# Optimization experiments

Measured on AMD Instinct MI355X. Metric: run time of the kernel, lower is better.

## Reference

```python
import jax, jax.numpy as jnp
import numpy as np

H = 64
EPS = 1e-5


def _lstm_layer(x, w_ih, w_hh, b_ih, b_hh):
    """Single LSTM layer, batch_first input x: [B, T, I]. PyTorch gate order i,f,g,o."""
    B, T, _ = x.shape
    # precompute input contributions for all timesteps: [B, T, 4H]
    xw = jnp.einsum('bti,gi->btg', x, w_ih) + (b_ih + b_hh)
    xw = jnp.swapaxes(xw, 0, 1)  # [T, B, 4H] for scan over time

    def step(carry, xw_t):
        h, c = carry
        gates = xw_t + h @ w_hh.T  # [B, 4H]
        i, f, g, o = jnp.split(gates, 4, axis=-1)
        i = jax.nn.sigmoid(i)
        f = jax.nn.sigmoid(f)
        g = jnp.tanh(g)
        o = jax.nn.sigmoid(o)
        c = f * c + i * g
        h = o * jnp.tanh(c)
        return (h, c), h

    h0 = jnp.zeros((B, H), x.dtype)
    (_, _), hs = jax.lax.scan(step, (h0, h0), xw)
    return jnp.swapaxes(hs, 0, 1)  # [B, T, H]


def setup_inputs() -> dict:
    key = jax.random.key(0)
    ks = jax.random.split(key, 16)
    B, T, F = 4096, 256, 32
    s = 1.0 / np.sqrt(H)  # PyTorch LSTM init scale
    inp = {
        'x': jax.random.normal(ks[0], (B, T, F), jnp.float32),
        'w_ih0': jax.random.uniform(ks[1], (4 * H, F), jnp.float32, -s, s),
        'w_hh0': jax.random.uniform(ks[2], (4 * H, H), jnp.float32, -s, s),
        'b_ih0': jax.random.uniform(ks[3], (4 * H,), jnp.float32, -s, s),
        'b_hh0': jax.random.uniform(ks[4], (4 * H,), jnp.float32, -s, s),
        'w_ih1': jax.random.uniform(ks[5], (4 * H, H), jnp.float32, -s, s),
        'w_hh1': jax.random.uniform(ks[6], (4 * H, H), jnp.float32, -s, s),
        'b_ih1': jax.random.uniform(ks[7], (4 * H,), jnp.float32, -s, s),
        'b_hh1': jax.random.uniform(ks[8], (4 * H,), jnp.float32, -s, s),
        'ln_g': jnp.ones((H,), jnp.float32),
        'ln_b': jnp.zeros((H,), jnp.float32),
        'w1': jax.random.uniform(ks[9], (64, H), jnp.float32, -s, s),
        'b1': jax.random.uniform(ks[10], (64,), jnp.float32, -s, s),
        'w2': jax.random.uniform(ks[11], (1, 64), jnp.float32, -0.125, 0.125),
        'b2': jax.random.uniform(ks[12], (1,), jnp.float32, -0.125, 0.125),
    }
    return inp


def reference(x, w_ih0, w_hh0, b_ih0, b_hh0, w_ih1, w_hh1, b_ih1, b_hh1,
              ln_g, ln_b, w1, b1, w2, b2):
    out0 = _lstm_layer(x, w_ih0, w_hh0, b_ih0, b_hh0)      # [B, T, H]
    out1 = _lstm_layer(out0, w_ih1, w_hh1, b_ih1, b_hh1)   # [B, T, H]
    last = out1[:, -1, :]                                   # [B, H]
    # LayerNorm
    mu = jnp.mean(last, axis=-1, keepdims=True)
    var = jnp.mean(jnp.square(last - mu), axis=-1, keepdims=True)
    ln = (last - mu) * jax.lax.rsqrt(var + EPS) * ln_g + ln_b
    # MLP head
    h = jax.nn.relu(ln @ w1.T + b1)
    y = h @ w2.T + b2                                       # [B, 1]
    return y[:, 0]
```

## Files before the change

### kernel.cpp

```cpp
#include <hip/hip_runtime.h>

#define TSEQ 256
#define FIN  32
#define HID  64

#define LOG2E    1.4426950408889634f
#define TWOLOG2E 2.8853900817779268f

typedef _Float16 f16x8 __attribute__((ext_vector_type(8)));
typedef __fp16   h16x2 __attribute__((ext_vector_type(2)));
typedef float    f32x4 __attribute__((ext_vector_type(4)));

#if __has_builtin(__builtin_amdgcn_exp2f)
__device__ __forceinline__ float fast_exp2(float x) { return __builtin_amdgcn_exp2f(x); }
#else
extern "C" __device__ float __ocml_native_exp2_f32(float);
__device__ __forceinline__ float fast_exp2(float x) { return __ocml_native_exp2_f32(x); }
#endif

#define BAR_LDS() do { asm volatile("s_waitcnt lgkmcnt(0)" ::: "memory"); \
                       __builtin_amdgcn_s_barrier(); } while (0)

__device__ __forceinline__ float wsum(float v) {
    #pragma unroll
    for (int off = 32; off > 0; off >>= 1) v += __shfl_xor(v, off, 64);
    return v;
}

__device__ __forceinline__ float lstm_cell(const f32x4 g, float& c) {
    float ei = fast_exp2(g[0]);
    float ef = fast_exp2(g[1]);
    float yg = fast_exp2(g[2]);
    float eo = fast_exp2(g[3]);
    float t1 = 1.0f + ei;
    float t2 = 1.0f + ef;
    float p  = t1 * (yg + 1.0f);
    float r  = __builtin_amdgcn_rcpf(p * t2);
    float ig = (yg - 1.0f) * t2 * r;
    float sf = p * r;
    c = fmaf(sf, c, ig);
    float cc = __builtin_amdgcn_fmed3f(c, -15.0f, 15.0f);
    float yc = fast_exp2(TWOLOG2E * cc);
    return (yc - 1.0f) * __builtin_amdgcn_rcpf((1.0f + eo) * (yc + 1.0f));
}

__global__ __launch_bounds__(1024, 4)
void lstm_fused(const float* __restrict__ x,
                const float* __restrict__ w_ih0, const float* __restrict__ w_hh0,
                const float* __restrict__ b_ih0, const float* __restrict__ b_hh0,
                const float* __restrict__ w_ih1, const float* __restrict__ w_hh1,
                const float* __restrict__ b_ih1, const float* __restrict__ b_hh1,
                const float* __restrict__ ln_g, const float* __restrict__ ln_b,
                const float* __restrict__ w1, const float* __restrict__ b1,
                const float* __restrict__ w2, const float* __restrict__ b2,
                float* __restrict__ out)
{
    __shared__ __align__(16) _Float16 H0[2][16][72];
    __shared__ __align__(16) _Float16 H1[2][16][72];
    __shared__ __align__(16) float HF[16][68];
    __shared__ __align__(16) float LNB[16][64];

    const int tid  = threadIdx.x;
    const int wave = tid >> 6;
    const int lane = tid & 63;
    const int q    = lane >> 4;
    const int lm   = lane & 15;
    const int q8   = q * 8;
    const int b0   = blockIdx.x * 16;

    const bool isA = wave < 8;
    const int  wt  = wave & 7;
    const int  T0  = 2 * wt, T1 = T0 + 1;
    const int  np0  = T0 * 16 + lm;
    const int  np1  = T1 * 16 + lm;
    const int  row0 = (np0 & 3) * 64 + (np0 >> 2);
    const int  row1 = (np1 & 3) * 64 + (np1 >> 2);
    const int  d0 = T0 * 4 + q;
    const int  d1 = T1 * 4 + q;
    const float wsc = ((lm & 3) == 2) ? TWOLOG2E : -LOG2E;

    f16x8 wf[8];
    f32x4 bias0, bias1;
    if (isA) {
        const float* p0 = w_ih0 + row0 * FIN + q8;
        const float* p1 = w_hh0 + row0 * HID + q8;
        const float* p2 = w_hh0 + row0 * HID + 32 + q8;
        const float* p3 = w_ih0 + row1 * FIN + q8;
        const float* p4 = w_hh0 + row1 * HID + q8;
        const float* p5 = w_hh0 + row1 * HID + 32 + q8;
        #pragma unroll
        for (int j = 0; j < 8; ++j) {
            wf[0][j] = (_Float16)(wsc * p0[j]);
            wf[1][j] = (_Float16)(wsc * p1[j]);
            wf[2][j] = (_Float16)(wsc * p2[j]);
            wf[3][j] = (_Float16)(wsc * p3[j]);
            wf[4][j] = (_Float16)(wsc * p4[j]);
            wf[5][j] = (_Float16)(wsc * p5[j]);
        }
        #pragma unroll
        for (int r = 0; r < 4; ++r) {
            const float s = (r == 2) ? TWOLOG2E : -LOG2E;
            bias0[r] = s * (b_ih0[r * 64 + d0] + b_hh0[r * 64 + d0]);
            bias1[r] = s * (b_ih0[r * 64 + d1] + b_hh0[r * 64 + d1]);
        }
    } else {
        const float* p0 = w_ih1 + row0 * HID + q8;
        const float* p1 = w_ih1 + row0 * HID + 32 + q8;
        const float* p2 = w_hh1 + row0 * HID + q8;
        const float* p3 = w_hh1 + row0 * HID + 32 + q8;
        const float* p4 = w_ih1 + row1 * HID + q8;
        const float* p5 = w_ih1 + row1 * HID + 32 + q8;
        const float* p6 = w_hh1 + row1 * HID + q8;
        const float* p7 = w_hh1 + row1 * HID + 32 + q8;
        #pragma unroll
        for (int j = 0; j < 8; ++j) {
            wf[0][j] = (_Float16)(wsc * p0[j]);
            wf[1][j] = (_Float16)(wsc * p1[j]);
            wf[2][j] = (_Float16)(wsc * p2[j]);
            wf[3][j] = (_Float16)(wsc * p3[j]);
            wf[4][j] = (_Float16)(wsc * p4[j]);
            wf[5][j] = (_Float16)(wsc * p5[j]);
            wf[6][j] = (_Float16)(wsc * p6[j]);
            wf[7][j] = (_Float16)(wsc * p7[j]);
        }
        #pragma unroll
        for (int r = 0; r < 4; ++r) {
            const float s = (r == 2) ? TWOLOG2E : -LOG2E;
            bias0[r] = s * (b_ih1[r * 64 + d0] + b_hh1[r * 64 + d0]);
            bias1[r] = s * (b_ih1[r * 64 + d1] + b_hh1[r * 64 + d1]);
        }
    }

    const float* xp = x + (size_t)(b0 + lm) * TSEQ * FIN + q8;
    f32x4 xfa, xfb;
    if (isA) {
        xfa = *reinterpret_cast<const f32x4*>(xp);
        xfb = *reinterpret_cast<const f32x4*>(xp + 4);
    }

    for (int i = tid; i < 2 * 16 * 72; i += 1024) {
        ((_Float16*)H0)[i] = (_Float16)0.0f;
        ((_Float16*)H1)[i] = (_Float16)0.0f;
    }
    float c0a = 0.0f, c0b = 0.0f, c1a = 0.0f, c1b = 0.0f;
    float lastB0 = 0.0f, lastB1 = 0.0f;
    __syncthreads();

#define MFMA __builtin_amdgcn_mfma_f32_16x16x32_f16
#define INTERVAL(P, DO_A, DO_B, DO_XL, XI)                                          \
    {                                                                               \
        if (isA) {                                                                  \
            f16x8 xcur;                                                             \
            {                                                                       \
                h16x2 c0_ = __builtin_amdgcn_cvt_pkrtz(xfa[0], xfa[1]);             \
                h16x2 c1_ = __builtin_amdgcn_cvt_pkrtz(xfa[2], xfa[3]);             \
                h16x2 c2_ = __builtin_amdgcn_cvt_pkrtz(xfb[0], xfb[1]);             \
                h16x2 c3_ = __builtin_amdgcn_cvt_pkrtz(xfb[2], xfb[3]);             \
                xcur[0] = (_Float16)c0_[0]; xcur[1] = (_Float16)c0_[1];             \
                xcur[2] = (_Float16)c1_[0]; xcur[3] = (_Float16)c1_[1];             \
                xcur[4] = (_Float16)c2_[0]; xcur[5] = (_Float16)c2_[1];             \
                xcur[6] = (_Float16)c3_[0]; xcur[7] = (_Float16)c3_[1];             \
            }                                                                       \
            if (DO_XL) {                                                            \
                xfa = *reinterpret_cast<const f32x4*>(xp + (size_t)(XI) * FIN);     \
                xfb = *reinterpret_cast<const f32x4*>(xp + (size_t)(XI) * FIN + 4); \
            }                                                                       \
            if (DO_A) {                                                             \
                f32x4 a0 = bias0, a1 = bias1;                                       \
                  \
                a0 = MFMA(wf[0], xcur, a0, 0, 0, 0);                                \
                a1 = MFMA(wf[3], xcur, a1, 0, 0, 0);                                \
                f16x8 rh0a = *reinterpret_cast<const f16x8*>(&H0[(P) ^ 1][lm][q8]);      \
                f16x8 rh0b = *reinterpret_cast<const f16x8*>(&H0[(P) ^ 1][lm][32 + q8]); \
                a0 = MFMA(wf[1], rh0a, a0, 0, 0, 0);                                \
                a1 = MFMA(wf[4], rh0a, a1, 0, 0, 0);                                \
                a0 = MFMA(wf[2], rh0b, a0, 0, 0, 0);                                \
                a1 = MFMA(wf[5], rh0b, a1, 0, 0, 0);                                \
                float hv0 = lstm_cell(a0, c0a);                                     \
                float hv1 = lstm_cell(a1, c0b);                                     \
                H0[P][lm][d0] = (_Float16)hv0;                                      \
                H0[P][lm][d1] = (_Float16)hv1;                                      \
            }                                                                       \
        } else if (DO_B) {                                                          \
                           \
            f16x8 rh0a = *reinterpret_cast<const f16x8*>(&H0[(P) ^ 1][lm][q8]);      \
            f16x8 rh0b = *reinterpret_cast<const f16x8*>(&H0[(P) ^ 1][lm][32 + q8]); \
            f32x4 a0 = bias0, a1 = bias1;                                           \
            a0 = MFMA(wf[0], rh0a, a0, 0, 0, 0);                                    \
            a1 = MFMA(wf[4], rh0a, a1, 0, 0, 0);                                    \
            a0 = MFMA(wf[1], rh0b, a0, 0, 0, 0);                                    \
            a1 = MFMA(wf[5], rh0b, a1, 0, 0, 0);                                    \
            f16x8 rh1a = *reinterpret_cast<const f16x8*>(&H1[P][lm][q8]);            \
            f16x8 rh1b = *reinterpret_cast<const f16x8*>(&H1[P][lm][32 + q8]);       \
            a0 = MFMA(wf[2], rh1a, a0, 0, 0, 0);                                    \
            a1 = MFMA(wf[6], rh1a, a1, 0, 0, 0);                                    \
            a0 = MFMA(wf[3], rh1b, a0, 0, 0, 0);                                    \
            a1 = MFMA(wf[7], rh1b, a1, 0, 0, 0);                                    \
            float hv0 = lstm_cell(a0, c1a);                                         \
            float hv1 = lstm_cell(a1, c1b);                                         \
            H1[(P) ^ 1][lm][d0] = (_Float16)hv0;                                    \
            H1[(P) ^ 1][lm][d1] = (_Float16)hv1;                                    \
            lastB0 = hv0; lastB1 = hv1;                                             \
        }                                                                           \
        BAR_LDS();                                                                  \
    }

    INTERVAL(0, true, false, true, 1)

    #pragma unroll 1
    for (int ii = 0; ii < 127; ++ii) {
        const int i1 = 2 * ii + 1;
        INTERVAL(1, true, true, true, i1 + 1)
        INTERVAL(0, true, true, true, i1 + 2)
    }

    INTERVAL(1, true, true, false, 0)
    INTERVAL(0, false, true, false, 0)

#undef INTERVAL
#undef MFMA

    if (!isA) {
        HF[lm][d0] = lastB0;
        HF[lm][d1] = lastB1;
    }
    __syncthreads();

    const float lngv = ln_g[lane], lnbv = ln_b[lane];
    const float b1v = b1[lane], w2v = w2[lane];
    const float* w1row = w1 + lane * 64;
    {
        float v  = HF[wave][lane];
        float mu = wsum(v) * (1.0f / 64.0f);
        float dv = v - mu;
        float var = wsum(dv * dv) * (1.0f / 64.0f);
        float ln = dv * rsqrtf(var + 1e-5f) * lngv + lnbv;
        LNB[wave][lane] = ln;
        float s = b1v;
        #pragma unroll
        for (int dd = 0; dd < 64; ++dd)
            s = fmaf(LNB[wave][dd], w1row[dd], s);
        s = fmaxf(s, 0.0f);
        float y = wsum(s * w2v);
        if (lane == 0) out[b0 + wave] = y + b2[0];
    }
}

extern "C" void kernel_launch(void* const* d_in, const int* in_sizes, int n_in,
                              void* d_out, int out_size, void* d_ws, size_t ws_size,
                              hipStream_t stream) {
    const float* x     = (const float*)d_in[0];
    const float* w_ih0 = (const float*)d_in[1];
    const float* w_hh0 = (const float*)d_in[2];
    const float* b_ih0 = (const float*)d_in[3];
    const float* b_hh0 = (const float*)d_in[4];
    const float* w_ih1 = (const float*)d_in[5];
    const float* w_hh1 = (const float*)d_in[6];
    const float* b_ih1 = (const float*)d_in[7];
    const float* b_hh1 = (const float*)d_in[8];
    const float* ln_g  = (const float*)d_in[9];
    const float* ln_b  = (const float*)d_in[10];
    const float* w1    = (const float*)d_in[11];
    const float* b1    = (const float*)d_in[12];
    const float* w2    = (const float*)d_in[13];
    const float* b2    = (const float*)d_in[14];
    lstm_fused<<<dim3(256), dim3(1024), 0, stream>>>(
        x, w_ih0, w_hh0, b_ih0, b_hh0,
        w_ih1, w_hh1, b_ih1, b_hh1,
        ln_g, ln_b, w1, b1, w2, b2, (float*)d_out);
}
```

Baseline: 365.4 us.

## Halve block to 512 threads with each wave computing four gate tiles

Reduces each block from 16 to 8 waves (4 per LSTM layer), so every wave now owns four 16-column output tiles instead of two, holding 16 f16x8 weight fragments and four cell states in registers. Fewer waves join each per-timestep barrier, which is meant to cut synchronisation cost and give each wave more independent MFMA chains to hide latency. The trade-off is a longer serial per-wave workload on the recurrent critical path, higher register pressure, and less parallelism per block with the grid size unchanged. The LayerNorm/MLP epilogue now loops so each wave handles two batch rows.

```diff
diff --git a/kernel.cpp b/kernel.cpp
--- a/kernel.cpp
+++ b/kernel.cpp
@@ -44,7 +44,7 @@
     return (yc - 1.0f) * __builtin_amdgcn_rcpf((1.0f + eo) * (yc + 1.0f));
 }
 
-__global__ __launch_bounds__(1024, 4)
+__global__ __launch_bounds__(512, 2)
 void lstm_fused(const float* __restrict__ x,
                 const float* __restrict__ w_ih0, const float* __restrict__ w_hh0,
                 const float* __restrict__ b_ih0, const float* __restrict__ b_hh0,
@@ -68,66 +68,55 @@
     const int q8   = q * 8;
     const int b0   = blockIdx.x * 16;
 
-    const bool isA = wave < 8;
-    const int  wt  = wave & 7;
-    const int  T0  = 2 * wt, T1 = T0 + 1;
-    const int  np0  = T0 * 16 + lm;
-    const int  np1  = T1 * 16 + lm;
-    const int  row0 = (np0 & 3) * 64 + (np0 >> 2);
-    const int  row1 = (np1 & 3) * 64 + (np1 >> 2);
-    const int  d0 = T0 * 4 + q;
-    const int  d1 = T1 * 4 + q;
+    const bool isA = wave < 4;
+    const int  wt  = wave & 3;
+    const int rbase = (lm & 3) * 64 + (lm >> 2);
+    const int dq0   = wt * 16 + q;
     const float wsc = ((lm & 3) == 2) ? TWOLOG2E : -LOG2E;
 
-    f16x8 wf[8];
-    f32x4 bias0, bias1;
+    f16x8 wf[16];
+    f32x4 biasv[4];
     if (isA) {
-        const float* p0 = w_ih0 + row0 * FIN + q8;
-        const float* p1 = w_hh0 + row0 * HID + q8;
-        const float* p2 = w_hh0 + row0 * HID + 32 + q8;
-        const float* p3 = w_ih0 + row1 * FIN + q8;
-        const float* p4 = w_hh0 + row1 * HID + q8;
-        const float* p5 = w_hh0 + row1 * HID + 32 + q8;
         #pragma unroll
-        for (int j = 0; j < 8; ++j) {
-            wf[0][j] = (_Float16)(wsc * p0[j]);
-            wf[1][j] = (_Float16)(wsc * p1[j]);
-            wf[2][j] = (_Float16)(wsc * p2[j]);
-            wf[3][j] = (_Float16)(wsc * p3[j]);
-            wf[4][j] = (_Float16)(wsc * p4[j]);
-            wf[5][j] = (_Float16)(wsc * p5[j]);
-        }
-        #pragma unroll
-        for (int r = 0; r < 4; ++r) {
-            const float s = (r == 2) ? TWOLOG2E : -LOG2E;
-            bias0[r] = s * (b_ih0[r * 64 + d0] + b_hh0[r * 64 + d0]);
-            bias1[r] = s * (b_ih0[r * 64 + d1] + b_hh0[r * 64 + d1]);
+        for (int t = 0; t < 4; ++t) {
+            const int row = rbase + wt * 16 + t * 4;
+            const float* p0 = w_ih0 + row * FIN + q8;
+            const float* p1 = w_hh0 + row * HID + q8;
+            const float* p2 = p1 + 32;
+            #pragma unroll
+            for (int j = 0; j < 8; ++j) {
+                wf[t * 3 + 0][j] = (_Float16)(wsc * p0[j]);
+                wf[t * 3 + 1][j] = (_Float16)(wsc * p1[j]);
+                wf[t * 3 + 2][j] = (_Float16)(wsc * p2[j]);
+            }
+            const int d = dq0 + t * 4;
+            #pragma unroll
+            for (int r = 0; r < 4; ++r) {
+                const float s = (r == 2) ? TWOLOG2E : -LOG2E;
+                biasv[t][r] = s * (b_ih0[r * 64 + d] + b_hh0[r * 64 + d]);
+            }
         }
     } else {
-        const float* p0 = w_ih1 + row0 * HID + q8;
-        const float* p1 = w_ih1 + row0 * HID + 32 + q8;
-        const float* p2 = w_hh1 + row0 * HID + q8;
-        const float* p3 = w_hh1 + row0 * HID + 32 + q8;
-        const float* p4 = w_ih1 + row1 * HID + q8;
-        const float* p5 = w_ih1 + row1 * HID + 32 + q8;
-        const float* p6 = w_hh1 + row1 * HID + q8;
-        const float* p7 = w_hh1 + row1 * HID + 32 + q8;
         #pragma unroll
-        for (int j = 0; j < 8; ++j) {
-            wf[0][j] = (_Float16)(wsc * p0[j]);
-            wf[1][j] = (_Float16)(wsc * p1[j]);
-            wf[2][j] = (_Float16)(wsc * p2[j]);
-            wf[3][j] = (_Float16)(wsc * p3[j]);
-            wf[4][j] = (_Float16)(wsc * p4[j]);
-            wf[5][j] = (_Float16)(wsc * p5[j]);
-            wf[6][j] = (_Float16)(wsc * p6[j]);
-            wf[7][j] = (_Float16)(wsc * p7[j]);
-        }
-        #pragma unroll
-        for (int r = 0; r < 4; ++r) {
-            const float s = (r == 2) ? TWOLOG2E : -LOG2E;
-            bias0[r] = s * (b_ih1[r * 64 + d0] + b_hh1[r * 64 + d0]);
-            bias1[r] = s * (b_ih1[r * 64 + d1] + b_hh1[r * 64 + d1]);
+        for (int t = 0; t < 4; ++t) {
+            const int row = rbase + wt * 16 + t * 4;
+            const float* p0 = w_ih1 + row * HID + q8;
+            const float* p1 = p0 + 32;
+            const float* p2 = w_hh1 + row * HID + q8;
+            const float* p3 = p2 + 32;
+            #pragma unroll
+            for (int j = 0; j < 8; ++j) {
+                wf[t * 4 + 0][j] = (_Float16)(wsc * p0[j]);
+                wf[t * 4 + 1][j] = (_Float16)(wsc * p1[j]);
+                wf[t * 4 + 2][j] = (_Float16)(wsc * p2[j]);
+                wf[t * 4 + 3][j] = (_Float16)(wsc * p3[j]);
+            }
+            const int d = dq0 + t * 4;
+            #pragma unroll
+            for (int r = 0; r < 4; ++r) {
+                const float s = (r == 2) ? TWOLOG2E : -LOG2E;
+                biasv[t][r] = s * (b_ih1[r * 64 + d] + b_hh1[r * 64 + d]);
+            }
         }
     }
 
@@ -138,12 +127,12 @@
         xfb = *reinterpret_cast<const f32x4*>(xp + 4);
     }
 
-    for (int i = tid; i < 2 * 16 * 72; i += 1024) {
+    for (int i = tid; i < 2 * 16 * 72; i += 512) {
         ((_Float16*)H0)[i] = (_Float16)0.0f;
         ((_Float16*)H1)[i] = (_Float16)0.0f;
     }
-    float c0a = 0.0f, c0b = 0.0f, c1a = 0.0f, c1b = 0.0f;
-    float lastB0 = 0.0f, lastB1 = 0.0f;
+    float cs0 = 0.0f, cs1 = 0.0f, cs2 = 0.0f, cs3 = 0.0f;
+    float lastB0 = 0.0f, lastB1 = 0.0f, lastB2 = 0.0f, lastB3 = 0.0f;
     __syncthreads();
 
 #define MFMA __builtin_amdgcn_mfma_f32_16x16x32_f16
@@ -166,41 +155,62 @@
                 xfb = *reinterpret_cast<const f32x4*>(xp + (size_t)(XI) * FIN + 4); \
             }                                                                       \
             if (DO_A) {                                                             \
-                f32x4 a0 = bias0, a1 = bias1;                                       \
-                  \
+                f32x4 a0 = biasv[0], a1 = biasv[1], a2 = biasv[2], a3 = biasv[3];   \
+                   \
                 a0 = MFMA(wf[0], xcur, a0, 0, 0, 0);                                \
                 a1 = MFMA(wf[3], xcur, a1, 0, 0, 0);                                \
+                a2 = MFMA(wf[6], xcur, a2, 0, 0, 0);                                \
+                a3 = MFMA(wf[9], xcur, a3, 0, 0, 0);                                \
                 f16x8 rh0a = *reinterpret_cast<const f16x8*>(&H0[(P) ^ 1][lm][q8]);      \
                 f16x8 rh0b = *reinterpret_cast<const f16x8*>(&H0[(P) ^ 1][lm][32 + q8]); \
-                a0 = MFMA(wf[1], rh0a, a0, 0, 0, 0);                                \
-                a1 = MFMA(wf[4], rh0a, a1, 0, 0, 0);                                \
-                a0 = MFMA(wf[2], rh0b, a0, 0, 0, 0);                                \
-                a1 = MFMA(wf[5], rh0b, a1, 0, 0, 0);                                \
-                float hv0 = lstm_cell(a0, c0a);                                     \
-                float hv1 = lstm_cell(a1, c0b);                                     \
-                H0[P][lm][d0] = (_Float16)hv0;                                      \
-                H0[P][lm][d1] = (_Float16)hv1;                                      \
+                a0 = MFMA(wf[1],  rh0a, a0, 0, 0, 0);                               \
+                a1 = MFMA(wf[4],  rh0a, a1, 0, 0, 0);                               \
+                a2 = MFMA(wf[7],  rh0a, a2, 0, 0, 0);                               \
+                a3 = MFMA(wf[10], rh0a, a3, 0, 0, 0);                               \
+                a0 = MFMA(wf[2],  rh0b, a0, 0, 0, 0);                               \
+                a1 = MFMA(wf[5],  rh0b, a1, 0, 0, 0);                               \
+                a2 = MFMA(wf[8],  rh0b, a2, 0, 0, 0);                               \
+                a3 = MFMA(wf[11], rh0b, a3, 0, 0, 0);                               \
+                float hv0 = lstm_cell(a0, cs0);                                     \
+                float hv1 = lstm_cell(a1, cs1);                                     \
+                float hv2 = lstm_cell(a2, cs2);                                     \
+                float hv3 = lstm_cell(a3, cs3);                                     \
+                H0[P][lm][dq0]      = (_Float16)hv0;                                \
+                H0[P][lm][dq0 + 4]  = (_Float16)hv1;                                \
+                H0[P][lm][dq0 + 8]  = (_Float16)hv2;                                \
+                H0[P][lm][dq0 + 12] = (_Float16)hv3;                                \
             }                                                                       \
         } else if (DO_B) {                                                          \
-                           \
             f16x8 rh0a = *reinterpret_cast<const f16x8*>(&H0[(P) ^ 1][lm][q8]);      \
             f16x8 rh0b = *reinterpret_cast<const f16x8*>(&H0[(P) ^ 1][lm][32 + q8]); \
-            f32x4 a0 = bias0, a1 = bias1;                                           \
-            a0 = MFMA(wf[0], rh0a, a0, 0, 0, 0);                                    \
-            a1 = MFMA(wf[4], rh0a, a1, 0, 0, 0);                                    \
-            a0 = MFMA(wf[1], rh0b, a0, 0, 0, 0);                                    \
-            a1 = MFMA(wf[5], rh0b, a1, 0, 0, 0);                                    \
+            f32x4 a0 = biasv[0], a1 = biasv[1], a2 = biasv[2], a3 = biasv[3];       \
+            a0 = MFMA(wf[0],  rh0a, a0, 0, 0, 0);                                   \
+            a1 = MFMA(wf[4],  rh0a, a1, 0, 0, 0);                                   \
+            a2 = MFMA(wf[8],  rh0a, a2, 0, 0, 0);                                   \
+            a3 = MFMA(wf[12], rh0a, a3, 0, 0, 0);                                   \
+            a0 = MFMA(wf[1],  rh0b, a0, 0, 0, 0);                                   \
+            a1 = MFMA(wf[5],  rh0b, a1, 0, 0, 0);                                   \
+            a2 = MFMA(wf[9],  rh0b, a2, 0, 0, 0);                                   \
+            a3 = MFMA(wf[13], rh0b, a3, 0, 0, 0);                                   \
             f16x8 rh1a = *reinterpret_cast<const f16x8*>(&H1[P][lm][q8]);            \
             f16x8 rh1b = *reinterpret_cast<const f16x8*>(&H1[P][lm][32 + q8]);       \
-            a0 = MFMA(wf[2], rh1a, a0, 0, 0, 0);                                    \
-            a1 = MFMA(wf[6], rh1a, a1, 0, 0, 0);                                    \
-            a0 = MFMA(wf[3], rh1b, a0, 0, 0, 0);                                    \
-            a1 = MFMA(wf[7], rh1b, a1, 0, 0, 0);                                    \
-            float hv0 = lstm_cell(a0, c1a);                                         \
-            float hv1 = lstm_cell(a1, c1b);                                         \
-            H1[(P) ^ 1][lm][d0] = (_Float16)hv0;                                    \
-            H1[(P) ^ 1][lm][d1] = (_Float16)hv1;                                    \
-            lastB0 = hv0; lastB1 = hv1;                                             \
+            a0 = MFMA(wf[2],  rh1a, a0, 0, 0, 0);                                   \
+            a1 = MFMA(wf[6],  rh1a, a1, 0, 0, 0);                                   \
+            a2 = MFMA(wf[10], rh1a, a2, 0, 0, 0);                                   \
+            a3 = MFMA(wf[14], rh1a, a3, 0, 0, 0);                                   \
+            a0 = MFMA(wf[3],  rh1b, a0, 0, 0, 0);                                   \
+            a1 = MFMA(wf[7],  rh1b, a1, 0, 0, 0);                                   \
+            a2 = MFMA(wf[11], rh1b, a2, 0, 0, 0);                                   \
+            a3 = MFMA(wf[15], rh1b, a3, 0, 0, 0);                                   \
+            float hv0 = lstm_cell(a0, cs0);                                         \
+            float hv1 = lstm_cell(a1, cs1);                                         \
+            float hv2 = lstm_cell(a2, cs2);                                         \
+            float hv3 = lstm_cell(a3, cs3);                                         \
+            H1[(P) ^ 1][lm][dq0]      = (_Float16)hv0;                              \
+            H1[(P) ^ 1][lm][dq0 + 4]  = (_Float16)hv1;                              \
+            H1[(P) ^ 1][lm][dq0 + 8]  = (_Float16)hv2;                              \
+            H1[(P) ^ 1][lm][dq0 + 12] = (_Float16)hv3;                              \
+            lastB0 = hv0; lastB1 = hv1; lastB2 = hv2; lastB3 = hv3;                 \
         }                                                                           \
         BAR_LDS();                                                                  \
     }
@@ -221,28 +231,31 @@
 #undef MFMA
 
     if (!isA) {
-        HF[lm][d0] = lastB0;
-        HF[lm][d1] = lastB1;
+        HF[lm][dq0]      = lastB0;
+        HF[lm][dq0 + 4]  = lastB1;
+        HF[lm][dq0 + 8]  = lastB2;
+        HF[lm][dq0 + 12] = lastB3;
     }
     __syncthreads();
 
     const float lngv = ln_g[lane], lnbv = ln_b[lane];
     const float b1v = b1[lane], w2v = w2[lane];
     const float* w1row = w1 + lane * 64;
-    {
-        float v  = HF[wave][lane];
+    #pragma unroll
+    for (int rr = wave; rr < 16; rr += 8) {
+        float v  = HF[rr][lane];
         float mu = wsum(v) * (1.0f / 64.0f);
         float dv = v - mu;
         float var = wsum(dv * dv) * (1.0f / 64.0f);
         float ln = dv * rsqrtf(var + 1e-5f) * lngv + lnbv;
-        LNB[wave][lane] = ln;
+        LNB[rr][lane] = ln;
         float s = b1v;
         #pragma unroll
         for (int dd = 0; dd < 64; ++dd)
-            s = fmaf(LNB[wave][dd], w1row[dd], s);
+            s = fmaf(LNB[rr][dd], w1row[dd], s);
         s = fmaxf(s, 0.0f);
         float y = wsum(s * w2v);
-        if (lane == 0) out[b0 + wave] = y + b2[0];
+        if (lane == 0) out[b0 + rr] = y + b2[0];
     }
 }
 
@@ -264,7 +277,7 @@
     const float* b1    = (const float*)d_in[12];
     const float* w2    = (const float*)d_in[13];
     const float* b2    = (const float*)d_in[14];
-    lstm_fused<<<dim3(256), dim3(1024), 0, stream>>>(
+    lstm_fused<<<dim3(256), dim3(512), 0, stream>>>(
         x, w_ih0, w_hh0, b_ih0, b_hh0,
         w_ih1, w_hh1, b_ih1, b_hh1,
         ln_g, ln_b, w1, b1, w2, b2, (float*)d_out);
```

Result: no change. 361.9 us (-1.0%).
